# Performance work log

Hardware: AMD Instinct MI355X
Metric: run time of the kernel (lower is better)

## Reference

```python
import jax, jax.numpy as jnp
import numpy as np

N = 100000   # nodes
E = 3200000  # directed edges
F_IN = 128   # data.num_node_features
H = 16       # hidden
C = 2        # output classes (hard-coded in module)


def _glorot(key, fan_in, fan_out):
    s = jnp.sqrt(6.0 / (fan_in + fan_out)).astype(jnp.float32)
    return jax.random.uniform(key, (fan_in, fan_out), jnp.float32, -s, s)


def setup_inputs() -> dict:
    key = jax.random.key(0)
    ks = jax.random.split(key, 5)
    x = jax.random.normal(ks[0], (N, F_IN), jnp.float32)
    edge_index = jax.random.randint(ks[1], (2, E), 0, N, dtype=jnp.int64)
    return {
        "x": x,
        "edge_index": edge_index,
        "W1": _glorot(ks[2], F_IN, H), "b1": jnp.zeros((H,), jnp.float32),
        "W2": _glorot(ks[3], H, H),    "b2": jnp.zeros((H,), jnp.float32),
        "W3": _glorot(ks[4], H, C),    "b3": jnp.zeros((C,), jnp.float32),
    }


def _gcn_conv(x, W, b, src, dst, norm, n):
    # PyG GCNConv: linear transform, then normalized gather -> scatter-add, + bias
    h = x @ W                                   # [N, out]
    msg = h[src] * norm[:, None]                # [E+N, out] gather over source nodes
    out = jax.ops.segment_sum(msg, dst, num_segments=n)  # scatter-add at targets
    return out + b


def reference(x, edge_index, W1, b1, W2, b2, W3, b3):
    n = x.shape[0]
    loop = jnp.arange(n, dtype=edge_index.dtype)
    src = jnp.concatenate([edge_index[0], loop])  # add self-loops (PyG default)
    dst = jnp.concatenate([edge_index[1], loop])
    # symmetric normalization: deg^{-1/2}[src] * deg^{-1/2}[dst], deg = in-degree w/ self-loops
    deg = jax.ops.segment_sum(jnp.ones(src.shape, jnp.float32), dst, num_segments=n)
    dis = jnp.where(deg > 0, jax.lax.rsqrt(jnp.maximum(deg, 1.0)), 0.0)
    norm = dis[src] * dis[dst]
    # dropout is identity in eval mode
    h = jax.nn.relu(_gcn_conv(x, W1, b1, src, dst, norm, n))
    h = jax.nn.relu(_gcn_conv(h, W2, b2, src, dst, norm, n))
    h = _gcn_conv(h, W3, b3, src, dst, norm, n)
    return jax.nn.log_softmax(h, axis=1)
```

## Files before the change

kernel.cpp:

```cpp
#include <hip/hip_runtime.h>
#include <math.h>

#define NSB   512
#define BSH   8
#define BKN   256
#define ESMAX 6272
#define TPB   8

typedef _Float16 h8  __attribute__((ext_vector_type(8)));
typedef _Float16 h2v __attribute__((ext_vector_type(2)));


__global__ void k_scan1(const int* __restrict__ in, int* __restrict__ out,
                        int* __restrict__ bsum, int n) {
    __shared__ int sd[256];
    int base = blockIdx.x * 2048 + threadIdx.x * 8;
    int v[8];
    int ts = 0;
#pragma unroll
    for (int j = 0; j < 8; j++) {
        int idx = base + j;
        v[j] = ts;
        ts += (idx < n) ? in[idx] : 0;
    }
    sd[threadIdx.x] = ts;
    __syncthreads();
    for (int ofs = 1; ofs < 256; ofs <<= 1) {
        int t = (threadIdx.x >= (unsigned)ofs) ? sd[threadIdx.x - ofs] : 0;
        __syncthreads();
        sd[threadIdx.x] += t;
        __syncthreads();
    }
    int excl = (threadIdx.x == 0) ? 0 : sd[threadIdx.x - 1];
#pragma unroll
    for (int j = 0; j < 8; j++) {
        int idx = base + j;
        if (idx < n) out[idx] = excl + v[j];
    }
    if (threadIdx.x == 255) bsum[blockIdx.x] = sd[255];
}

__global__ void k_scan2(int* __restrict__ bsum, int nb) {
    __shared__ int sd[256];
    int orig = (threadIdx.x < (unsigned)nb) ? bsum[threadIdx.x] : 0;
    sd[threadIdx.x] = orig;
    __syncthreads();
    for (int ofs = 1; ofs < 256; ofs <<= 1) {
        int t = (threadIdx.x >= (unsigned)ofs) ? sd[threadIdx.x - ofs] : 0;
        __syncthreads();
        sd[threadIdx.x] += t;
        __syncthreads();
    }
    if (threadIdx.x < (unsigned)nb) bsum[threadIdx.x] = sd[threadIdx.x] - orig;
}

__global__ void k_scan3(int* __restrict__ out, const int* __restrict__ bsum, int n) {
    int i = blockIdx.x * blockDim.x + threadIdx.x;
    if (i < n) out[i] += bsum[i >> 11];
}


__global__ void k_hist(const int* __restrict__ dst, int* __restrict__ hist,
                       int e, int nbuck, int es) {
    __shared__ int h[512];
    for (int i = threadIdx.x; i < 512; i += blockDim.x) h[i] = 0;
    __syncthreads();
    int lo = blockIdx.x * es;
    int hi = min(lo + es, e);
    for (int i = lo + threadIdx.x; i < hi; i += blockDim.x)
        atomicAdd(&h[dst[i] >> BSH], 1);
    __syncthreads();
    for (int i = threadIdx.x; i < nbuck; i += blockDim.x)
        hist[(size_t)i * gridDim.x + blockIdx.x] = h[i];
}

__global__ void k_bucket(const int* __restrict__ src, const int* __restrict__ dst,
                         const int* __restrict__ offs, unsigned* __restrict__ col,
                         int e, int nbuck, int es) {
    __shared__ unsigned sorted[ESMAX];
    __shared__ unsigned char sbuck[ESMAX];
    __shared__ int lc[512], lsc[512], lofE[512], lcur[512], soff[512];
    int tid = threadIdx.x;
    lc[tid] = 0;
    if (tid < nbuck) soff[tid] = offs[(size_t)tid * gridDim.x + blockIdx.x];
    __syncthreads();
    int lo = blockIdx.x * es;
    int hi = min(lo + es, e);
    for (int i = lo + tid; i < hi; i += 512)
        atomicAdd(&lc[dst[i] >> BSH], 1);
    __syncthreads();
    lsc[tid] = lc[tid];
    __syncthreads();
    for (int ofs = 1; ofs < 512; ofs <<= 1) {
        int t = (tid >= ofs) ? lsc[tid - ofs] : 0;
        __syncthreads();
        lsc[tid] += t;
        __syncthreads();
    }
    int excl = (tid == 0) ? 0 : lsc[tid - 1];
    lofE[tid] = excl;
    lcur[tid] = excl;
    __syncthreads();
    for (int i = lo + tid; i < hi; i += 512) {
        int d = dst[i];
        int b = d >> BSH;
        int p = atomicAdd(&lcur[b], 1);
        sorted[p] = ((unsigned)src[i] << BSH) | (unsigned)(d & (BKN - 1));
        sbuck[p] = (unsigned char)(b & 255);
    }
    __syncthreads();
    int cnt_ = hi - lo;
    int split = (nbuck > 256) ? lofE[256] : 0x7fffffff;
    for (int i = tid; i < cnt_; i += 512) {
        int b = sbuck[i] | ((i >= split) ? 256 : 0);
        col[soff[b] + (i - lofE[b])] = sorted[i];
    }
}

__global__ void k_sort(const unsigned* __restrict__ col, const int* __restrict__ offs,
                       int* __restrict__ col2, int* __restrict__ rs,
                       float* __restrict__ dis, int n, int e, int nbuck) {
    __shared__ int cnt[BKN];
    __shared__ int sd[BKN];
    __shared__ int cur[BKN];
    int tid = threadIdx.x;
    int b = blockIdx.x;
    int lo = offs[(size_t)b * NSB];
    int hi = (b + 1 < nbuck) ? offs[(size_t)(b + 1) * NSB] : e;
    if (tid < BKN) cnt[tid] = 0;
    __syncthreads();
    for (int i = lo + tid; i < hi; i += 512)
        atomicAdd(&cnt[col[i] & (BKN - 1u)], 1);
    __syncthreads();
    if (tid < BKN) sd[tid] = cnt[tid];
    __syncthreads();
    for (int ofs = 1; ofs < BKN; ofs <<= 1) {
        int t = (tid < BKN && tid >= ofs) ? sd[tid - ofs] : 0;
        __syncthreads();
        if (tid < BKN) sd[tid] += t;
        __syncthreads();
    }
    if (tid < BKN) {
        int excl = (tid == 0) ? 0 : sd[tid - 1];
        cur[tid] = lo + excl;
        int node = (b << BSH) + tid;
        if (node < n) {
            rs[node] = lo + excl;
            dis[node] = rsqrtf((float)(cnt[tid] + 1));
        }
    }
    if (b == 0 && tid == 0) rs[n] = e;
    __syncthreads();
    for (int i = lo + tid; i < hi; i += 512) {
        unsigned v = col[i];
        int pos = atomicAdd(&cur[v & (BKN - 1u)], 1);
        col2[pos] = (int)(v >> BSH);
    }
}


__global__ void k_linear1s(const float* __restrict__ x, const float* __restrict__ W,
                           const float* __restrict__ dis, _Float16* __restrict__ hs,
                           int n, int ntiles) {
    __shared__ float sWT[16 * 132];
    __shared__ float sx[16 * 132];
    int tid = threadIdx.x;
    for (int i = tid; i < 2048; i += 256) {
        int k = i >> 4, c = i & 15;
        sWT[c * 132 + k] = W[i];
    }
    int tile0 = blockIdx.x * TPB;
    const float4* xg4 = (const float4*)x;
    for (int tile = tile0; tile < tile0 + TPB && tile < ntiles; tile++) {
        int nodeBase = tile * 16;
        __syncthreads();
        for (int i = tid; i < 512; i += 256) {
            int nl = i >> 5, k4 = i & 31;
            int nd = nodeBase + nl;
            float4 v = make_float4(0.f, 0.f, 0.f, 0.f);
            if (nd < n) v = xg4[(size_t)nd * 32 + k4];
            *((float4*)(sx + nl * 132 + k4 * 4)) = v;
        }
        __syncthreads();
        int nl = tid >> 4, c = tid & 15;
        int node = nodeBase + nl;
        const float4* xr = (const float4*)(sx + nl * 132);
        const float4* wr = (const float4*)(sWT + c * 132);
        float acc = 0.f;
#pragma unroll
        for (int k4 = 0; k4 < 32; k4++) {
            float4 xv = xr[k4];
            float4 wv = wr[k4];
            acc += xv.x * wv.x + xv.y * wv.y + xv.z * wv.z + xv.w * wv.w;
        }
        if (node < n)
            hs[(size_t)node * 16 + c] = (_Float16)(acc * dis[node]);
    }
}


__global__ void k_pullA(const _Float16* __restrict__ hs, const int* __restrict__ rs,
                        const int* __restrict__ col2, const float* __restrict__ dis,
                        const float* __restrict__ bb, const float* __restrict__ W,
                        _Float16* __restrict__ hsOut, int n) {
    __shared__ float sW[256];
    __shared__ float sb[16];
    if (threadIdx.x < 256) sW[threadIdx.x] = W[threadIdx.x];
    if (threadIdx.x < 16) sb[threadIdx.x] = bb[threadIdx.x];
    __syncthreads();
    int t = blockIdx.x * blockDim.x + threadIdx.x;
    int node = t >> 2, sub = t & 3;
    int q = sub & 1, half = sub >> 1;
    if (node >= n) return;
    const h8* H = (const h8*)hs;
    float acc[8];
    if (half == 0) {
        h8 self = H[(size_t)node * 2 + q];
#pragma unroll
        for (int j = 0; j < 8; j++) acc[j] = (float)self[j];
    } else {
#pragma unroll
        for (int j = 0; j < 8; j++) acc[j] = 0.f;
    }
    int b = rs[node], e2 = rs[node + 1];
    int mid = b + ((e2 - b) >> 1);
    int i  = half ? mid : b;
    int en = half ? e2  : mid;
    for (; i + 3 < en; i += 4) {
        int s0 = col2[i], s1 = col2[i + 1], s2 = col2[i + 2], s3 = col2[i + 3];
        h8 v0 = H[(size_t)s0 * 2 + q];
        h8 v1 = H[(size_t)s1 * 2 + q];
        h8 v2 = H[(size_t)s2 * 2 + q];
        h8 v3 = H[(size_t)s3 * 2 + q];
#pragma unroll
        for (int j = 0; j < 8; j++)
            acc[j] += (float)v0[j] + (float)v1[j] + (float)v2[j] + (float)v3[j];
    }
    for (; i < en; i++) {
        h8 v = H[(size_t)col2[i] * 2 + q];
#pragma unroll
        for (int j = 0; j < 8; j++) acc[j] += (float)v[j];
    }
#pragma unroll
    for (int j = 0; j < 8; j++) acc[j] += __shfl_xor(acc[j], 2);
    float d = dis[node];
    float va[16];
#pragma unroll
    for (int j = 0; j < 8; j++) {
        int k = q * 8 + j;
        float v = acc[j] * d + sb[k];
        v = v > 0.f ? v : 0.f;
        float other = __shfl_xor(v, 1);
        va[j]     = q ? other : v;
        va[8 + j] = q ? v : other;
    }
    if (half == 0) {
        h8 o;
#pragma unroll
        for (int j = 0; j < 8; j++) {
            int c = q * 8 + j;
            float s = 0.f;
#pragma unroll
            for (int k = 0; k < 16; k++) s += va[k] * sW[k * 16 + c];
            o[j] = (_Float16)(s * d);
        }
        ((h8*)hsOut)[(size_t)node * 2 + q] = o;
    }
}


__global__ void k_pullB(const _Float16* __restrict__ hs, const int* __restrict__ rs,
                        const int* __restrict__ col2, const float* __restrict__ dis,
                        const float* __restrict__ bb, const float* __restrict__ W,
                        _Float16* __restrict__ hs2, int n) {
    __shared__ float sW[32];
    __shared__ float sb[16];
    if (threadIdx.x < 32) sW[threadIdx.x] = W[threadIdx.x];
    if (threadIdx.x < 16) sb[threadIdx.x] = bb[threadIdx.x];
    __syncthreads();
    int t = blockIdx.x * blockDim.x + threadIdx.x;
    int node = t >> 2, sub = t & 3;
    int q = sub & 1, half = sub >> 1;
    if (node >= n) return;
    const h8* H = (const h8*)hs;
    float acc[8];
    if (half == 0) {
        h8 self = H[(size_t)node * 2 + q];
#pragma unroll
        for (int j = 0; j < 8; j++) acc[j] = (float)self[j];
    } else {
#pragma unroll
        for (int j = 0; j < 8; j++) acc[j] = 0.f;
    }
    int b = rs[node], e2 = rs[node + 1];
    int mid = b + ((e2 - b) >> 1);
    int i  = half ? mid : b;
    int en = half ? e2  : mid;
    for (; i + 3 < en; i += 4) {
        int s0 = col2[i], s1 = col2[i + 1], s2 = col2[i + 2], s3 = col2[i + 3];
        h8 v0 = H[(size_t)s0 * 2 + q];
        h8 v1 = H[(size_t)s1 * 2 + q];
        h8 v2 = H[(size_t)s2 * 2 + q];
        h8 v3 = H[(size_t)s3 * 2 + q];
#pragma unroll
        for (int j = 0; j < 8; j++)
            acc[j] += (float)v0[j] + (float)v1[j] + (float)v2[j] + (float)v3[j];
    }
    for (; i < en; i++) {
        h8 v = H[(size_t)col2[i] * 2 + q];
#pragma unroll
        for (int j = 0; j < 8; j++) acc[j] += (float)v[j];
    }
#pragma unroll
    for (int j = 0; j < 8; j++) acc[j] += __shfl_xor(acc[j], 2);
    float d = dis[node];
    float p0 = 0.f, p1 = 0.f;
#pragma unroll
    for (int j = 0; j < 8; j++) {
        int k = q * 8 + j;
        float v = acc[j] * d + sb[k];
        v = v > 0.f ? v : 0.f;
        p0 += v * sW[k * 2 + 0];
        p1 += v * sW[k * 2 + 1];
    }
    p0 += __shfl_xor(p0, 1);
    p1 += __shfl_xor(p1, 1);
    if (sub == 0) {
        h2v o;
        o[0] = (_Float16)(p0 * d);
        o[1] = (_Float16)(p1 * d);
        ((h2v*)hs2)[node] = o;
    }
}


__global__ void k_pull2lsm(const _Float16* __restrict__ hs2, const int* __restrict__ rs,
                           const int* __restrict__ col2, const float* __restrict__ dis,
                           const float* __restrict__ b3, float* __restrict__ out, int n) {
    int t = blockIdx.x * blockDim.x + threadIdx.x;
    int node = t >> 1, half = t & 1;
    if (node >= n) return;
    const h2v* H = (const h2v*)hs2;
    float a0 = 0.f, a1 = 0.f;
    if (half == 0) {
        h2v self = H[node];
        a0 = (float)self[0]; a1 = (float)self[1];
    }
    int b = rs[node], e2 = rs[node + 1];
    int mid = b + ((e2 - b) >> 1);
    int i  = half ? mid : b;
    int en = half ? e2  : mid;
    for (; i + 3 < en; i += 4) {
        h2v v0 = H[col2[i]];
        h2v v1 = H[col2[i + 1]];
        h2v v2 = H[col2[i + 2]];
        h2v v3 = H[col2[i + 3]];
        a0 += (float)v0[0] + (float)v1[0] + (float)v2[0] + (float)v3[0];
        a1 += (float)v0[1] + (float)v1[1] + (float)v2[1] + (float)v3[1];
    }
    for (; i < en; i++) {
        h2v v = H[col2[i]];
        a0 += (float)v[0];
        a1 += (float)v[1];
    }
    a0 += __shfl_xor(a0, 1);
    a1 += __shfl_xor(a1, 1);
    if (half == 0) {
        float d = dis[node];
        float z0 = a0 * d + b3[0];
        float z1 = a1 * d + b3[1];
        float m = fmaxf(z0, z1);
        float l = m + logf(expf(z0 - m) + expf(z1 - m));
        float2 o = {z0 - l, z1 - l};
        ((float2*)out)[node] = o;
    }
}


extern "C" void kernel_launch(void* const* d_in, const int* in_sizes, int n_in,
                              void* d_out, int out_size, void* d_ws, size_t ws_size,
                              hipStream_t stream) {
    const float* x  = (const float*)d_in[0];
    const int*   ei = (const int*)d_in[1];
    const float* W1 = (const float*)d_in[2];
    const float* b1 = (const float*)d_in[3];
    const float* W2 = (const float*)d_in[4];
    const float* b2 = (const float*)d_in[5];
    const float* W3 = (const float*)d_in[6];
    const float* b3 = (const float*)d_in[7];
    float* out = (float*)d_out;

    const int N = in_sizes[0] / 128;
    const int E = in_sizes[1] / 2;
    const int* src = ei;
    const int* dst = ei + E;

    const int NBUCK = (N + BKN - 1) >> BSH;
    const int M = NBUCK * NSB;
    const int ES = (E + NSB - 1) / NSB;

    char* ws = (char*)d_ws;
    size_t off = 0;
    auto alloc = [&](size_t bytes) {
        void* p = ws + off;
        off += (bytes + 255) & ~(size_t)255;
        return p;
    };
    int*       hist = (int*)alloc((size_t)M * sizeof(int));
    int*       offs = (int*)alloc((size_t)M * sizeof(int));
    int*       bsum = (int*)alloc(256 * sizeof(int));
    unsigned*  col  = (unsigned*)alloc((size_t)E * sizeof(unsigned));
    int*       col2 = (int*)alloc((size_t)E * sizeof(int));
    int*       rs   = (int*)alloc((size_t)(N + 1) * sizeof(int));
    float*     dis  = (float*)alloc((size_t)N * sizeof(float));
    _Float16*  hsA  = (_Float16*)alloc((size_t)N * 16 * sizeof(_Float16));
    _Float16*  hsB  = (_Float16*)alloc((size_t)N * 16 * sizeof(_Float16));
    _Float16*  hs2  = (_Float16*)alloc((size_t)N * 2 * sizeof(_Float16));

    const int B = 256;
    auto g = [&](long long work) { return (int)((work + B - 1) / B); };
    const int NBS = (M + 2047) / 2048;

    k_hist<<<NSB, B, 0, stream>>>(dst, hist, E, NBUCK, ES);
    k_scan1<<<NBS, 256, 0, stream>>>(hist, offs, bsum, M);
    k_scan2<<<1, 256, 0, stream>>>(bsum, NBS);
    k_scan3<<<g(M), B, 0, stream>>>(offs, bsum, M);
    k_bucket<<<NSB, 512, 0, stream>>>(src, dst, offs, col, E, NBUCK, ES);
    k_sort<<<NBUCK, 512, 0, stream>>>(col, offs, col2, rs, dis, N, E, NBUCK);

    const int NTILES = (N + 15) / 16;
    k_linear1s<<<(NTILES + TPB - 1) / TPB, B, 0, stream>>>(x, W1, dis, hsA, N, NTILES);

    k_pullA<<<g((long long)N * 4), B, 0, stream>>>(hsA, rs, col2, dis, b1, W2, hsB, N);

    k_pullB<<<g((long long)N * 4), B, 0, stream>>>(hsB, rs, col2, dis, b2, W3, hs2, N);

    k_pull2lsm<<<g((long long)N * 2), B, 0, stream>>>(hs2, rs, col2, dis, b3, out, N);
}
```

Measured before the change: 257.1 us.

## Fold scan fixup into consumers, reuse histogram, rewrite first linear layer

Drops the k_scan3 pass by adding the block-sum offset where k_bucket and k_sort read offsets. k_bucket now loads its per-block bucket counts from the histogram instead of re-counting dst with shared atomics, which removes a full read of dst. k_linear1s is rewritten so each thread keeps a 16x4 slice of W in registers, reads x straight from global with float4 loads, reduces across k-groups with shuffles and writes packed half4 outputs. The register-held weights raise register pressure, and the offset fixup now costs an extra bsum load at each use.

Result: no change. 259.5 us (+0.9%).

```diff
diff --git a/kernel.cpp b/kernel.cpp
--- a/kernel.cpp
+++ b/kernel.cpp
@@ -5,9 +5,9 @@
 #define BSH   8
 #define BKN   256
 #define ESMAX 6272
-#define TPB   8
 
 typedef _Float16 h8  __attribute__((ext_vector_type(8)));
+typedef _Float16 h4  __attribute__((ext_vector_type(4)));
 typedef _Float16 h2v __attribute__((ext_vector_type(2)));
 
 
@@ -54,11 +54,6 @@
     if (threadIdx.x < (unsigned)nb) bsum[threadIdx.x] = sd[threadIdx.x] - orig;
 }
 
-__global__ void k_scan3(int* __restrict__ out, const int* __restrict__ bsum, int n) {
-    int i = blockIdx.x * blockDim.x + threadIdx.x;
-    if (i < n) out[i] += bsum[i >> 11];
-}
-
 
 __global__ void k_hist(const int* __restrict__ dst, int* __restrict__ hist,
                        int e, int nbuck, int es) {
@@ -75,20 +70,23 @@
 }
 
 __global__ void k_bucket(const int* __restrict__ src, const int* __restrict__ dst,
-                         const int* __restrict__ offs, unsigned* __restrict__ col,
+                         const int* __restrict__ hist, const int* __restrict__ offs,
+                         const int* __restrict__ bsum, unsigned* __restrict__ col,
                          int e, int nbuck, int es) {
     __shared__ unsigned sorted[ESMAX];
     __shared__ unsigned char sbuck[ESMAX];
     __shared__ int lc[512], lsc[512], lofE[512], lcur[512], soff[512];
     int tid = threadIdx.x;
-    lc[tid] = 0;
-    if (tid < nbuck) soff[tid] = offs[(size_t)tid * gridDim.x + blockIdx.x];
+    if (tid < nbuck) {
+        size_t idx = (size_t)tid * gridDim.x + blockIdx.x;
+        lc[tid] = hist[idx];
+        soff[tid] = offs[idx] + bsum[idx >> 11];
+    } else {
+        lc[tid] = 0;
+    }
     __syncthreads();
     int lo = blockIdx.x * es;
     int hi = min(lo + es, e);
-    for (int i = lo + tid; i < hi; i += 512)
-        atomicAdd(&lc[dst[i] >> BSH], 1);
-    __syncthreads();
     lsc[tid] = lc[tid];
     __syncthreads();
     for (int ofs = 1; ofs < 512; ofs <<= 1) {
@@ -118,15 +116,21 @@
 }
 
 __global__ void k_sort(const unsigned* __restrict__ col, const int* __restrict__ offs,
-                       int* __restrict__ col2, int* __restrict__ rs,
-                       float* __restrict__ dis, int n, int e, int nbuck) {
+                       const int* __restrict__ bsum, int* __restrict__ col2,
+                       int* __restrict__ rs, float* __restrict__ dis,
+                       int n, int e, int nbuck) {
     __shared__ int cnt[BKN];
     __shared__ int sd[BKN];
     __shared__ int cur[BKN];
     int tid = threadIdx.x;
     int b = blockIdx.x;
-    int lo = offs[(size_t)b * NSB];
-    int hi = (b + 1 < nbuck) ? offs[(size_t)(b + 1) * NSB] : e;
+    size_t i0 = (size_t)b * NSB;
+    int lo = offs[i0] + bsum[i0 >> 11];
+    int hi = e;
+    if (b + 1 < nbuck) {
+        size_t i1 = (size_t)(b + 1) * NSB;
+        hi = offs[i1] + bsum[i1 >> 11];
+    }
     if (tid < BKN) cnt[tid] = 0;
     __syncthreads();
     for (int i = lo + tid; i < hi; i += 512)
@@ -159,42 +163,55 @@
 }
 
 
-__global__ void k_linear1s(const float* __restrict__ x, const float* __restrict__ W,
-                           const float* __restrict__ dis, _Float16* __restrict__ hs,
-                           int n, int ntiles) {
-    __shared__ float sWT[16 * 132];
-    __shared__ float sx[16 * 132];
+__global__ __launch_bounds__(512) void k_linear1s(
+        const float* __restrict__ x, const float* __restrict__ W,
+        const float* __restrict__ dis, _Float16* __restrict__ hs, int n) {
+    __shared__ float sW[2048];
     int tid = threadIdx.x;
-    for (int i = tid; i < 2048; i += 256) {
-        int k = i >> 4, c = i & 15;
-        sWT[c * 132 + k] = W[i];
-    }
-    int tile0 = blockIdx.x * TPB;
-    const float4* xg4 = (const float4*)x;
-    for (int tile = tile0; tile < tile0 + TPB && tile < ntiles; tile++) {
-        int nodeBase = tile * 16;
-        __syncthreads();
-        for (int i = tid; i < 512; i += 256) {
-            int nl = i >> 5, k4 = i & 31;
-            int nd = nodeBase + nl;
-            float4 v = make_float4(0.f, 0.f, 0.f, 0.f);
-            if (nd < n) v = xg4[(size_t)nd * 32 + k4];
-            *((float4*)(sx + nl * 132 + k4 * 4)) = v;
+    for (int i = tid; i < 2048; i += 512) sW[i] = W[i];
+    __syncthreads();
+    int cg = tid & 3;
+    int kg = (tid >> 2) & 7;
+    int nl = tid >> 5;
+    float wr[16][4];
+#pragma unroll
+    for (int j = 0; j < 16; j++)
+#pragma unroll
+        for (int cc = 0; cc < 4; cc++)
+            wr[j][cc] = sW[(kg * 16 + j) * 16 + cg * 4 + cc];
+    int nodeBase = blockIdx.x * 128 + nl;
+    for (int it = 0; it < 8; it++) {
+        int node = nodeBase + it * 16;
+        float a0 = 0.f, a1 = 0.f, a2 = 0.f, a3 = 0.f;
+        if (node < n) {
+            const float4* xr = (const float4*)(x + (size_t)node * 128 + kg * 16);
+#pragma unroll
+            for (int j4 = 0; j4 < 4; j4++) {
+                float4 xv = xr[j4];
+                float xs0 = xv.x, xs1 = xv.y, xs2 = xv.z, xs3 = xv.w;
+                int j = j4 * 4;
+                a0 += xs0 * wr[j][0] + xs1 * wr[j+1][0] + xs2 * wr[j+2][0] + xs3 * wr[j+3][0];
+                a1 += xs0 * wr[j][1] + xs1 * wr[j+1][1] + xs2 * wr[j+2][1] + xs3 * wr[j+3][1];
+                a2 += xs0 * wr[j][2] + xs1 * wr[j+1][2] + xs2 * wr[j+2][2] + xs3 * wr[j+3][2];
+                a3 += xs0 * wr[j][3] + xs1 * wr[j+1][3] + xs2 * wr[j+2][3] + xs3 * wr[j+3][3];
+            }
         }
-        __syncthreads();
-        int nl = tid >> 4, c = tid & 15;
-        int node = nodeBase + nl;
-        const float4* xr = (const float4*)(sx + nl * 132);
-        const float4* wr = (const float4*)(sWT + c * 132);
-        float acc = 0.f;
-#pragma unroll
-        for (int k4 = 0; k4 < 32; k4++) {
-            float4 xv = xr[k4];
-            float4 wv = wr[k4];
-            acc += xv.x * wv.x + xv.y * wv.y + xv.z * wv.z + xv.w * wv.w;
+#pragma unroll
+        for (int m = 4; m <= 16; m <<= 1) {
+            a0 += __shfl_xor(a0, m);
+            a1 += __shfl_xor(a1, m);
+            a2 += __shfl_xor(a2, m);
+            a3 += __shfl_xor(a3, m);
         }
-        if (node < n)
-            hs[(size_t)node * 16 + c] = (_Float16)(acc * dis[node]);
+        if (kg == 0 && node < n) {
+            float d = dis[node];
+            h4 o;
+            o[0] = (_Float16)(a0 * d);
+            o[1] = (_Float16)(a1 * d);
+            o[2] = (_Float16)(a2 * d);
+            o[3] = (_Float16)(a3 * d);
+            *((h4*)(hs + (size_t)node * 16 + cg * 4)) = o;
+        }
     }
 }
 
@@ -424,12 +441,10 @@
     k_hist<<<NSB, B, 0, stream>>>(dst, hist, E, NBUCK, ES);
     k_scan1<<<NBS, 256, 0, stream>>>(hist, offs, bsum, M);
     k_scan2<<<1, 256, 0, stream>>>(bsum, NBS);
-    k_scan3<<<g(M), B, 0, stream>>>(offs, bsum, M);
-    k_bucket<<<NSB, 512, 0, stream>>>(src, dst, offs, col, E, NBUCK, ES);
-    k_sort<<<NBUCK, 512, 0, stream>>>(col, offs, col2, rs, dis, N, E, NBUCK);
-
-    const int NTILES = (N + 15) / 16;
-    k_linear1s<<<(NTILES + TPB - 1) / TPB, B, 0, stream>>>(x, W1, dis, hsA, N, NTILES);
+    k_bucket<<<NSB, 512, 0, stream>>>(src, dst, hist, offs, bsum, col, E, NBUCK, ES);
+    k_sort<<<NBUCK, 512, 0, stream>>>(col, offs, bsum, col2, rs, dis, N, E, NBUCK);
+
+    k_linear1s<<<(N + 127) / 128, 512, 0, stream>>>(x, W1, dis, hsA, N);
 
     k_pullA<<<g((long long)N * 4), B, 0, stream>>>(hsA, rs, col2, dis, b1, W2, hsB, N);
 
```
